# Kernel optimization log

Measured on AMD Instinct MI355X. Metric: run time of the kernel, lower is better.

Reference implementation:

```python
import jax, jax.numpy as jnp
import numpy as np
from jax import lax

N = 163840      # total nodes
E = 2621440     # total edges (avg degree 16)
B = 4096        # number of graphs / batch
F_XD = 78       # node feature dim
L_XT = 735      # cell-line sequence length (gives 2944 after conv/pool stack)


def _params(key):
    ks = jax.random.split(key, 26)
    s = 0.05
    rn = lambda k, sh: (jax.random.normal(k, sh, jnp.float32) * s)
    p = {}
    p['W1'], p['b1'] = rn(ks[0], (78, 78)), rn(ks[1], (78,))
    p['W2'], p['b2'] = rn(ks[2], (78, 156)), rn(ks[3], (156,))
    p['W3'], p['b3'] = rn(ks[4], (156, 312)), rn(ks[5], (312,))
    p['Wg1'], p['bg1'] = rn(ks[6], (312, 1024)), rn(ks[7], (1024,))
    p['Wg2'], p['bg2'] = rn(ks[8], (1024, 128)), rn(ks[9], (128,))
    p['k1'], p['kb1'] = rn(ks[10], (32, 1, 8)), rn(ks[11], (32,))
    p['k2'], p['kb2'] = rn(ks[12], (64, 32, 8)), rn(ks[13], (64,))
    p['k3'], p['kb3'] = rn(ks[14], (128, 64, 8)), rn(ks[15], (128,))
    p['Wxt'], p['bxt'] = rn(ks[16], (2944, 128)), rn(ks[17], (128,))
    p['Wf1'], p['bf1'] = rn(ks[18], (256, 1024)), rn(ks[19], (1024,))
    p['Wf2'], p['bf2'] = rn(ks[20], (1024, 128)), rn(ks[21], (128,))
    p['Wo'], p['bo'] = rn(ks[22], (128, 1)), rn(ks[23], (1,))
    return p


def setup_inputs() -> dict:
    key = jax.random.key(0)
    k0, k1, k2, kp = jax.random.split(key, 4)
    inp = {
        'x': jax.random.normal(k0, (N, F_XD), jnp.float32),
        'edge_index': jax.random.randint(k1, (2, E), 0, N),
        'batch': jnp.arange(N) // (N // B),  # contiguous graph ids, 40 nodes/graph
        'xo': jax.random.normal(k2, (B, 1, L_XT), jnp.float32),
    }
    inp.update(_params(kp))
    return inp


def _forward(x, xo, W1, b1, W2, b2, W3, b3, Wg1, bg1, Wg2, bg2,
             k1, kb1, k2, kb2, k3, kb3, Wxt, bxt, Wf1, bf1, Wf2, bf2, Wo, bo,
             edge_index, batch):
    src, dst = edge_index[0], edge_index[1]
    # GCN symmetric norm with self-loops: deg = in-degree + 1
    deg = jax.ops.segment_sum(jnp.ones(src.shape[0], x.dtype), dst, num_segments=N) + 1.0
    dinv = lax.rsqrt(deg)
    enorm = (dinv[src] * dinv[dst])[:, None]     # [E,1]
    selfn = (dinv * dinv)[:, None]               # [N,1]

    def gcn(h, W, b):
        h = h @ W
        agg = jax.ops.segment_sum(h[src] * enorm, dst, num_segments=N)
        return agg + h * selfn + b

    h = jax.nn.relu(gcn(x, W1, b1))
    h = jax.nn.relu(gcn(h, W2, b2))
    h = jax.nn.relu(gcn(h, W3, b3))
    g = jax.ops.segment_max(h, batch, num_segments=B)   # global max pool -> [B,312]
    g = jax.nn.relu(g @ Wg1 + bg1)
    g = g @ Wg2 + bg2                                   # [B,128] (dropout = eval no-op)

    def conv1d(v, w, b):
        y = lax.conv_general_dilated(v, w, (1,), 'VALID',
                                     dimension_numbers=('NCH', 'OIH', 'NCH'))
        return y + b[None, :, None]

    def pool3(v):
        return lax.reduce_window(v, -jnp.inf, lax.max, (1, 1, 3), (1, 1, 3), 'VALID')

    t = pool3(jax.nn.relu(conv1d(xo, k1, kb1)))   # [B,32,242]
    t = pool3(jax.nn.relu(conv1d(t, k2, kb2)))    # [B,64,78]
    t = pool3(jax.nn.relu(conv1d(t, k3, kb3)))    # [B,128,23]
    t = t.reshape(B, -1) @ Wxt + bxt              # [B,128]

    c = jnp.concatenate([g, t], axis=1)           # [B,256]
    c = jax.nn.relu(c @ Wf1 + bf1)
    c = jax.nn.relu(c @ Wf2 + bf2)
    return c @ Wo + bo                            # [B,1]


def reference(x, edge_index, batch, xo, W1, b1, W2, b2, W3, b3, Wg1, bg1,
              Wg2, bg2, k1, kb1, k2, kb2, k3, kb3, Wxt, bxt, Wf1, bf1,
              Wf2, bf2, Wo, bo):
    return _forward(x, xo, W1, b1, W2, b2, W3, b3, Wg1, bg1, Wg2, bg2,
                    k1, kb1, k2, kb2, k3, kb3, Wxt, bxt, Wf1, bf1, Wf2, bf2,
                    Wo, bo, edge_index, batch)
```

## Files before the change

kernel.cpp:

```cpp
#include <hip/hip_runtime.h>
#include <hip/hip_bf16.h>

#define N_NODES 163840
#define N_EDGES 2621440
#define NB      4096

typedef __hip_bfloat16 bf16;
typedef __attribute__((ext_vector_type(8))) short short8;
typedef __attribute__((ext_vector_type(4))) float floatx4;

__device__ inline float tofloat(float v) { return v; }
__device__ inline float tofloat(bf16 v) { return __bfloat162float(v); }
__device__ inline void storev(float* p, float v) { *p = v; }
__device__ inline void storev(bf16* p, float v) { *p = __float2bfloat16(v); }
__device__ inline float s2f(short s) {
  union { unsigned u; float f; } cv;
  cv.u = ((unsigned)(unsigned short)s) << 16;
  return cv.f;
}
__device__ inline short f2s(float f) {
  bf16 b = __float2bfloat16(f);
  return *(short*)&b;
}


__global__ __launch_bounds__(256) void count_kernel(const int* __restrict__ ei,
                                                    int* __restrict__ indeg) {
  int e = blockIdx.x * 256 + threadIdx.x;
  if (e < N_EDGES) atomicAdd(&indeg[ei[N_EDGES + e]], 1);
}

__global__ __launch_bounds__(256) void scan1_kernel(const int* __restrict__ indeg,
                                                    int* __restrict__ rowstart,
                                                    int* __restrict__ bsums,
                                                    float* __restrict__ dinv) {
  __shared__ int s[256];
  int tid = threadIdx.x;
  int i = blockIdx.x * 256 + tid;
  int v = indeg[i];
  dinv[i] = rsqrtf((float)v + 1.0f);
  s[tid] = v;
  __syncthreads();
  for (int off = 1; off < 256; off <<= 1) {
    int x = (tid >= off) ? s[tid - off] : 0;
    __syncthreads();
    s[tid] += x;
    __syncthreads();
  }
  rowstart[i] = s[tid] - v;
  if (tid == 255) bsums[blockIdx.x] = s[255];
}

__global__ __launch_bounds__(640) void scan2_kernel(const int* __restrict__ bsums,
                                                    int* __restrict__ boffs,
                                                    int* __restrict__ rowstart) {
  __shared__ int s[640];
  int tid = threadIdx.x;
  int v = bsums[tid];
  s[tid] = v;
  __syncthreads();
  for (int off = 1; off < 640; off <<= 1) {
    int x = (tid >= off) ? s[tid - off] : 0;
    __syncthreads();
    s[tid] += x;
    __syncthreads();
  }
  boffs[tid] = s[tid] - v;
  if (tid == 639) rowstart[N_NODES] = s[639];
}

__global__ __launch_bounds__(256) void scan3_kernel(int* __restrict__ rowstart,
                                                    int* __restrict__ cursor,
                                                    const int* __restrict__ boffs) {
  int i = blockIdx.x * 256 + threadIdx.x;
  int v = rowstart[i] + boffs[blockIdx.x];
  rowstart[i] = v;
  cursor[i] = v;
}

__global__ __launch_bounds__(256) void scatter_kernel(const int* __restrict__ ei,
                                                      int* __restrict__ cursor,
                                                      int* __restrict__ csr_src) {
  int e = blockIdx.x * 256 + threadIdx.x;
  int lo = blockIdx.y * (N_NODES / 4);
  int hi = lo + (N_NODES / 4);
  if (e < N_EDGES) {
    int d = ei[N_EDGES + e];
    if (d >= lo && d < hi) {
      int pos = atomicAdd(&cursor[d], 1);
      csr_src[pos] = ei[e];
    }
  }
}

__global__ __launch_bounds__(256) void cast_scale_kernel(const float* __restrict__ x,
                                                         const float* __restrict__ dinv,
                                                         bf16* __restrict__ xb) {
  int i = blockIdx.x * 256 + threadIdx.x;
  if (i < N_NODES * 80) {
    int n = i / 80, f = i - n * 80;
    float v = (f < 78) ? x[n * 78 + f] * dinv[n] : 0.f;
    xb[i] = __float2bfloat16(v);
  }
}

__global__ __launch_bounds__(256) void agg80_kernel(const bf16* __restrict__ hs,
                                                    const float* __restrict__ dinv,
                                                    const int* __restrict__ rowstart,
                                                    const int* __restrict__ csr,
                                                    bf16* __restrict__ out) {
  int node = blockIdx.x * 4 + (threadIdx.x >> 6);
  int lane = threadIdx.x & 63;
  int grp = lane / 10;
  int sub = lane - grp * 10;
  bool active = grp < 6;
  int st = rowstart[node], en = rowstart[node + 1];
  int cnt = en - st + 1;
  float dn = dinv[node];
  float acc[8];
#pragma unroll
  for (int j = 0; j < 8; j++) acc[j] = 0.f;
  for (int e = 0; e < cnt; e += 6) {
    int ri = e + grp;
    bool valid = active && (ri < cnt);
    int cidx = st + ri;
    cidx = (cidx < en) ? cidx : 0;
    int row = (ri < cnt - 1) ? csr[cidx] : node;
    const short* rp = (const short*)hs + (size_t)row * 80 + sub * 8;
    short8 d = *(const short8*)rp;
    float m = valid ? 1.f : 0.f;
#pragma unroll
    for (int j = 0; j < 8; j++) acc[j] += m * s2f(d[j]);
  }
  short ob[8];
#pragma unroll
  for (int j = 0; j < 8; j++) {
    float v = acc[j];
    float t = 0.f;
#pragma unroll
    for (int g = 0; g < 6; g++) t += __shfl(v, sub + 10 * g);
    ob[j] = f2s(t * dn);
  }
  if (grp == 0) {
    short8 pk;
#pragma unroll
    for (int j = 0; j < 8; j++) pk[j] = ob[j];
    *(short8*)((short*)out + (size_t)node * 80 + sub * 8) = pk;
  }
}

__global__ __launch_bounds__(256) void agg192_kernel(const bf16* __restrict__ hs,
                                                     const float* __restrict__ dinv,
                                                     const int* __restrict__ rowstart,
                                                     const int* __restrict__ csr,
                                                     bf16* __restrict__ out) {
  int node = blockIdx.x * 4 + (threadIdx.x >> 6);
  int lane = threadIdx.x & 63;
  int grp = lane >> 3;
  int sub = lane & 7;
  int st = rowstart[node], en = rowstart[node + 1];
  int cnt = en - st + 1;
  float dn = dinv[node];
  float acc[3][8];
#pragma unroll
  for (int k = 0; k < 3; k++)
#pragma unroll
    for (int j = 0; j < 8; j++) acc[k][j] = 0.f;
  for (int e = 0; e < cnt; e += 8) {
    int ri = e + grp;
    bool valid = ri < cnt;
    int cidx = st + ri;
    cidx = (cidx < en) ? cidx : 0;
    int row = (ri < cnt - 1) ? csr[cidx] : node;
    const short* rp = (const short*)hs + (size_t)row * 192 + sub * 8;
    float m = valid ? 1.f : 0.f;
#pragma unroll
    for (int k = 0; k < 3; k++) {
      short8 d = *(const short8*)(rp + k * 64);
#pragma unroll
      for (int j = 0; j < 8; j++) acc[k][j] += m * s2f(d[j]);
    }
  }
#pragma unroll
  for (int k = 0; k < 3; k++) {
    short8 pk;
#pragma unroll
    for (int j = 0; j < 8; j++) {
      float v = acc[k][j];
      v += __shfl_xor(v, 8);
      v += __shfl_xor(v, 16);
      v += __shfl_xor(v, 32);
      pk[j] = f2s(v * dn);
    }
    if (grp == 0 && (k < 2 || sub < 4))
      *(short8*)((short*)out + (size_t)node * 160 + k * 64 + sub * 8) = pk;
  }
}

template <int NT, typename TC>
__global__ __launch_bounds__(256) void gemm_mfma_kernel(
    const bf16* __restrict__ A, const bf16* __restrict__ Bt,
    const float* __restrict__ bias, const float* __restrict__ rowScale,
    TC* __restrict__ C, int M, int Nc, int ncstore, int Ksteps, int lda,
    int kpad, int ldc, int coff, int doRelu) {
  int tid = threadIdx.x;
  int w = tid >> 6, lane = tid & 63;
  int quad = lane >> 4, l16 = lane & 15;
  int r0 = blockIdx.x * 64 + w * 16;
  int c0 = blockIdx.y * (NT * 16);
  floatx4 acc[NT];
#pragma unroll
  for (int t = 0; t < NT; t++) acc[t] = (floatx4){0.f, 0.f, 0.f, 0.f};
  const short* Ap = (const short*)A + (size_t)(r0 + l16) * lda + quad * 8;
  const short* Bp = (const short*)Bt + (size_t)(c0 + l16) * kpad + quad * 8;
  for (int s = 0; s < Ksteps; s++) {
    short8 a = *(const short8*)(Ap + s * 32);
#pragma unroll
    for (int t = 0; t < NT; t++) {
      short8 b = *(const short8*)(Bp + (size_t)t * 16 * kpad + s * 32);
      acc[t] = __builtin_amdgcn_mfma_f32_16x16x32_bf16(a, b, acc[t], 0, 0, 0);
    }
  }
#pragma unroll
  for (int t = 0; t < NT; t++) {
    int c = c0 + t * 16 + l16;
    if (c >= ncstore) continue;
    bool valid = c < Nc;
    float bb = (bias && valid) ? bias[c] : 0.f;
#pragma unroll
    for (int r = 0; r < 4; r++) {
      int row = r0 + quad * 4 + r;
      float v = valid ? acc[t][r] + bb : 0.f;
      if (doRelu) v = fmaxf(v, 0.f);
      if (rowScale) v *= rowScale[row];
      storev(&C[(size_t)row * ldc + coff + c], v);
    }
  }
}

__device__ inline void wtrans_one(const float* __restrict__ W, bf16* __restrict__ Bt,
                                  int K, int N, int Kpad, int idx) {
  int n = idx / Kpad, k = idx - n * Kpad;
  float v = (k < K && n < N) ? W[(size_t)k * N + n] : 0.f;
  Bt[idx] = __float2bfloat16(v);
}
template <int CI, int NCO>
__device__ inline void wprep_one(const float* __restrict__ kw, bf16* __restrict__ Wr,
                                 int idx) {
  int co = idx % NCO, k = idx / NCO;
  int dl = k / CI, ci = k % CI;
  Wr[idx] = __float2bfloat16(kw[(co * CI + ci) * 8 + dl]);
}
__global__ __launch_bounds__(256) void wprep_all_kernel(
    const float* k2, const float* k3, const float* W1, const float* W2,
    const float* W3, const float* Wg1, const float* Wg2, const float* Wxt,
    const float* Wf1, const float* Wf2, bf16* Wr2, bf16* Wr3, bf16* Btw1,
    bf16* Btw2, bf16* BtW3, bf16* Btg1, bf16* Btg2, bf16* Btxt, bf16* Btf1,
    bf16* Btf2, int* indeg) {
  int idx = blockIdx.x * 256 + threadIdx.x;
  if (idx < N_NODES) { indeg[idx] = 0; return; }
  idx -= N_NODES;
  if (idx < 16384) { wprep_one<32, 64>(k2, Wr2, idx); return; }
  idx -= 16384;
  if (idx < 65536) { wprep_one<64, 128>(k3, Wr3, idx); return; }
  idx -= 65536;
  if (idx < 7680) { wtrans_one(W1, Btw1, 78, 78, 96, idx); return; }
  idx -= 7680;
  if (idx < 15360) { wtrans_one(W2, Btw2, 78, 156, 96, idx); return; }
  idx -= 15360;
  if (idx < 51200) { wtrans_one(W3, BtW3, 156, 312, 160, idx); return; }
  idx -= 51200;
  if (idx < 327680) { wtrans_one(Wg1, Btg1, 312, 1024, 320, idx); return; }
  idx -= 327680;
  if (idx < 131072) { wtrans_one(Wg2, Btg2, 1024, 128, 1024, idx); return; }
  idx -= 131072;
  if (idx < 376832) {
    int o = idx / 2944, k = idx - o * 2944;
    int l = k >> 7, co = k & 127;
    Btxt[idx] = __float2bfloat16(Wxt[((size_t)(co * 23 + l)) * 128 + o]);
    return;
  }
  idx -= 376832;
  if (idx < 262144) { wtrans_one(Wf1, Btf1, 256, 1024, 256, idx); return; }
  idx -= 262144;
  if (idx < 131072) { wtrans_one(Wf2, Btf2, 1024, 128, 1024, idx); return; }
}
#define WPREP_TOTAL (N_NODES + 16384 + 65536 + 7680 + 15360 + 51200 + 327680 + 131072 + 376832 + 262144 + 131072)

__global__ __launch_bounds__(256) void gcn3_segmax_mfma_kernel(
    const bf16* __restrict__ agg2, const bf16* __restrict__ BtW3,
    const float* __restrict__ b3, bf16* __restrict__ g) {
  __shared__ __align__(16) bf16 a_lds[160 * 168];
  int tid = threadIdx.x;
  int w = tid >> 6, lane = tid & 63;
  int quad = lane >> 4, l16 = lane & 15;
  int g0 = blockIdx.x * 4;

  short8 bfrag[5][5];
  const short* Bp = (const short*)BtW3 + (size_t)(w * 80 + l16) * 160 + quad * 8;
#pragma unroll
  for (int nt = 0; nt < 5; nt++)
#pragma unroll
    for (int ks = 0; ks < 5; ks++)
      bfrag[nt][ks] = *(const short8*)(Bp + (size_t)nt * 16 * 160 + ks * 32);

  const bf16* src = agg2 + (size_t)g0 * 40 * 160;
  for (int i = tid; i < 160 * 160 / 8; i += 256) {
    int flat = i * 8;
    int row = flat / 160, k = flat - row * 160;
    *(short8*)&a_lds[row * 168 + k] = *(const short8*)&src[flat];
  }
  __syncthreads();

  float gmax[5][4];
#pragma unroll
  for (int nt = 0; nt < 5; nt++)
#pragma unroll
    for (int gi = 0; gi < 4; gi++) gmax[nt][gi] = -3.0e38f;

#pragma unroll
  for (int mt = 0; mt < 10; mt++) {
    floatx4 acc[5];
#pragma unroll
    for (int nt = 0; nt < 5; nt++) acc[nt] = (floatx4){0.f, 0.f, 0.f, 0.f};
#pragma unroll
    for (int ks = 0; ks < 5; ks++) {
      short8 a = *(const short8*)&a_lds[(16 * mt + l16) * 168 + ks * 32 + quad * 8];
#pragma unroll
      for (int nt = 0; nt < 5; nt++)
        acc[nt] = __builtin_amdgcn_mfma_f32_16x16x32_bf16(a, bfrag[nt][ks], acc[nt], 0, 0, 0);
    }
    int gl = (16 * mt + quad * 4) / 40;
#pragma unroll
    for (int nt = 0; nt < 5; nt++) {
      float m4 = fmaxf(fmaxf(acc[nt][0], acc[nt][1]), fmaxf(acc[nt][2], acc[nt][3]));
#pragma unroll
      for (int gi = 0; gi < 4; gi++)
        if (gl == gi) gmax[nt][gi] = fmaxf(gmax[nt][gi], m4);
    }
  }

#pragma unroll
  for (int nt = 0; nt < 5; nt++) {
#pragma unroll
    for (int gi = 0; gi < 4; gi++) {
      float v = gmax[nt][gi];
      v = fmaxf(v, __shfl_xor(v, 16));
      v = fmaxf(v, __shfl_xor(v, 32));
      gmax[nt][gi] = v;
    }
    int c = w * 80 + nt * 16 + l16;
    float bb = (c < 312) ? b3[c] : 0.f;
    float val = fmaxf(gmax[nt][quad] + bb, 0.f);
    g[(size_t)(g0 + quad) * 320 + c] = __float2bfloat16(val);
  }
}

__global__ __launch_bounds__(256) void conv12_kernel(const float* __restrict__ xo,
                                                     const float* __restrict__ k1,
                                                     const float* __restrict__ kb1,
                                                     const bf16* __restrict__ Wr2,
                                                     const float* __restrict__ kb2,
                                                     bf16* __restrict__ outp) {
  constexpr int LPAD = 248, MT = 15, LOUT = 78, G = 2, NCO = 64, CIP = 40;
  __shared__ __align__(16) bf16 lds_in[G * LPAD * CIP];
  __shared__ bf16 stg[4][MT * 16][16];
  __shared__ float xo_s[G][736];
  __shared__ float k1w[256];
  __shared__ float kb1s[32];
  int tid = threadIdx.x;
  int w = tid >> 6, lane = tid & 63;
  int quad = lane >> 4, l16 = lane & 15;
  int bg = blockIdx.x;
  int co0 = w * 16;

  short8 bfrag[8];
#pragma unroll
  for (int s = 0; s < 8; s++) {
#pragma unroll
    for (int j = 0; j < 8; j++) {
      int k = s * 32 + quad * 8 + j;
      bfrag[s][j] = ((const short*)Wr2)[k * NCO + co0 + l16];
    }
  }

  for (int i = tid; i < G * 735; i += 256)
    xo_s[i / 735][i % 735] = xo[(size_t)(bg * G + i / 735) * 735 + i % 735];
  k1w[tid] = k1[tid];
  if (tid < 32) kb1s[tid] = kb1[tid];
  __syncthreads();

  for (int idx = tid; idx < G * 242 * 32; idx += 256) {
    int g = idx / (242 * 32);
    int rem = idx - g * (242 * 32);
    int l = rem >> 5, co = rem & 31;
    int base = l * 3;
    float bs = kb1s[co];
    float a0 = bs, a1 = bs, a2 = bs;
#pragma unroll
    for (int k = 0; k < 8; k++) {
      float wv = k1w[co * 8 + k];
      a0 += wv * xo_s[g][base + k];
      a1 += wv * xo_s[g][base + 1 + k];
      a2 += wv * xo_s[g][base + 2 + k];
    }
    lds_in[(g * LPAD + l) * CIP + co] =
        __float2bfloat16(fmaxf(0.f, fmaxf(a0, fmaxf(a1, a2))));
  }
  for (int i = tid; i < G * 6 * 32; i += 256) {
    int g = i / (6 * 32);
    int rem = i - g * (6 * 32);
    int r = rem >> 5, c = rem & 31;
    lds_in[(g * LPAD + 242 + r) * CIP + c] = __float2bfloat16(0.f);
  }
  __syncthreads();

  for (int g = 0; g < G; g++) {
    const bf16* base = &lds_in[g * LPAD * CIP];
#pragma unroll
    for (int mt = 0; mt < MT; mt++) {
      floatx4 acc = {0.f, 0.f, 0.f, 0.f};
      int m = mt * 16 + l16;
#pragma unroll
      for (int s = 0; s < 8; s++) {
        int kg0 = s * 32 + quad * 8;
        int dl = kg0 >> 5;
        int ci0 = kg0 & 31;
        short8 a = *(const short8*)&base[(m + dl) * CIP + ci0];
        acc = __builtin_amdgcn_mfma_f32_16x16x32_bf16(a, bfrag[s], acc, 0, 0, 0);
      }
#pragma unroll
      for (int r = 0; r < 4; r++)
        stg[w][mt * 16 + quad * 4 + r][l16] = __float2bfloat16(acc[r]);
    }
    __syncthreads();
    float bias = kb2[co0 + l16];
    for (int it = lane; it < LOUT * 16; it += 64) {
      int l = it >> 4;
      float v0 = __bfloat162float(stg[w][3 * l][l16]);
      float v1 = __bfloat162float(stg[w][3 * l + 1][l16]);
      float v2 = __bfloat162float(stg[w][3 * l + 2][l16]);
      float v = fmaxf(fmaxf(v0, v1), v2) + bias;
      outp[((size_t)(bg * G + g) * LOUT + l) * NCO + co0 + l16] =
          __float2bfloat16(fmaxf(v, 0.f));
    }
    __syncthreads();
  }
}

template <int CI, int LIN, int LPAD, int MT, int LOUT, int G, int NCO>
__global__ __launch_bounds__(256) void convmfma_kernel(const bf16* __restrict__ in,
                                                       const bf16* __restrict__ Wr,
                                                       const float* __restrict__ kb,
                                                       bf16* __restrict__ outp) {
  constexpr int KSTEPS = 8 * CI / 32;
  constexpr int CIP = CI + 8;
  __shared__ __align__(16) bf16 lds_in[G * LPAD * CIP];
  __shared__ bf16 stg[4][MT * 16][16];
  int tid = threadIdx.x;
  int w = tid >> 6, lane = tid & 63;
  int quad = lane >> 4, l16 = lane & 15;
  int bg = blockIdx.x;
  int co0 = blockIdx.y * 64 + w * 16;

  short8 bfrag[KSTEPS];
#pragma unroll
  for (int s = 0; s < KSTEPS; s++) {
#pragma unroll
    for (int j = 0; j < 8; j++) {
      int k = s * 32 + quad * 8 + j;
      bfrag[s][j] = ((const short*)Wr)[k * NCO + co0 + l16];
    }
  }

  const bf16* gin = in + (size_t)bg * G * LIN * CI;
  constexpr int NELEM = G * LIN * CI;
  for (int i = tid; i < NELEM / 8; i += 256) {
    int flat = i * 8;
    int g = flat / (LIN * CI);
    int rem = flat - g * (LIN * CI);
    int row = rem / CI, ci = rem - row * CI;
    *(short8*)&lds_in[(g * LPAD + row) * CIP + ci] = *(const short8*)&gin[flat];
  }
  constexpr int PADE = G * (LPAD - LIN) * CIP;
  for (int i = tid; i < PADE / 8; i += 256) {
    int flat = i * 8;
    int g = flat / ((LPAD - LIN) * CIP);
    int rem = flat - g * ((LPAD - LIN) * CIP);
    short8 z = {0, 0, 0, 0, 0, 0, 0, 0};
    *(short8*)&lds_in[(g * LPAD + LIN) * CIP + rem] = z;
  }
  __syncthreads();

  for (int g = 0; g < G; g++) {
    const bf16* base = &lds_in[g * LPAD * CIP];
#pragma unroll
    for (int mt = 0; mt < MT; mt++) {
      floatx4 acc = {0.f, 0.f, 0.f, 0.f};
      int m = mt * 16 + l16;
#pragma unroll
      for (int s = 0; s < KSTEPS; s++) {
        int kg0 = s * 32 + quad * 8;
        int dl = kg0 / CI;
        int ci0 = kg0 % CI;
        short8 a = *(const short8*)&base[(m + dl) * CIP + ci0];
        acc = __builtin_amdgcn_mfma_f32_16x16x32_bf16(a, bfrag[s], acc, 0, 0, 0);
      }
#pragma unroll
      for (int r = 0; r < 4; r++)
        stg[w][mt * 16 + quad * 4 + r][l16] = __float2bfloat16(acc[r]);
    }
    __syncthreads();
    float bias = kb[co0 + l16];
    for (int it = lane; it < LOUT * 16; it += 64) {
      int l = it >> 4;
      float v0 = __bfloat162float(stg[w][3 * l][l16]);
      float v1 = __bfloat162float(stg[w][3 * l + 1][l16]);
      float v2 = __bfloat162float(stg[w][3 * l + 2][l16]);
      float v = fmaxf(fmaxf(v0, v1), v2) + bias;
      outp[((size_t)(bg * G + g) * LOUT + l) * NCO + co0 + l16] =
          __float2bfloat16(fmaxf(v, 0.f));
    }
    __syncthreads();
  }
}

__global__ __launch_bounds__(256) void final_kernel(const float* __restrict__ f2,
                                                    const float* __restrict__ Wo,
                                                    const float* __restrict__ bo,
                                                    float* __restrict__ out) {
  int wid = (blockIdx.x * blockDim.x + threadIdx.x) >> 6;
  int lane = threadIdx.x & 63;
  if (wid >= NB) return;
  float s = f2[wid * 128 + lane] * Wo[lane] + f2[wid * 128 + 64 + lane] * Wo[64 + lane];
  for (int o = 32; o > 0; o >>= 1) s += __shfl_down(s, o);
  if (lane == 0) out[wid] = s + bo[0];
}

extern "C" void kernel_launch(void* const* d_in, const int* in_sizes, int n_in,
                              void* d_out, int out_size, void* d_ws, size_t ws_size,
                              hipStream_t stream) {
  const float* x   = (const float*)d_in[0];
  const int*   ei  = (const int*)d_in[1];
  const float* xo  = (const float*)d_in[3];
  const float* W1  = (const float*)d_in[4];  const float* b1  = (const float*)d_in[5];
  const float* W2  = (const float*)d_in[6];  const float* b2  = (const float*)d_in[7];
  const float* W3  = (const float*)d_in[8];  const float* b3  = (const float*)d_in[9];
  const float* Wg1 = (const float*)d_in[10]; const float* bg1 = (const float*)d_in[11];
  const float* Wg2 = (const float*)d_in[12]; const float* bg2 = (const float*)d_in[13];
  const float* k1  = (const float*)d_in[14]; const float* kb1 = (const float*)d_in[15];
  const float* k2  = (const float*)d_in[16]; const float* kb2 = (const float*)d_in[17];
  const float* k3  = (const float*)d_in[18]; const float* kb3 = (const float*)d_in[19];
  const float* Wxt = (const float*)d_in[20]; const float* bxt = (const float*)d_in[21];
  const float* Wf1 = (const float*)d_in[22]; const float* bf1 = (const float*)d_in[23];
  const float* Wf2 = (const float*)d_in[24]; const float* bf2 = (const float*)d_in[25];
  const float* Wo  = (const float*)d_in[26]; const float* bo  = (const float*)d_in[27];
  float* out = (float*)d_out;

  char* ws = (char*)d_ws;
  size_t off = 0;
  auto alloc = [&](size_t bytes) -> void* {
    void* p = ws + off;
    off += (bytes + 255) & ~(size_t)255;
    return p;
  };

  int*   indeg   = (int*)alloc((size_t)N_NODES * 4);
  float* dinv    = (float*)alloc((size_t)N_NODES * 4);
  int*   rowstart= (int*)alloc((size_t)(N_NODES + 1) * 4);
  int*   cursor  = (int*)alloc((size_t)N_NODES * 4);
  int*   bsums   = (int*)alloc(640 * 4);
  int*   boffs   = (int*)alloc(640 * 4);
  int*   csr     = (int*)alloc((size_t)N_EDGES * 4 + 256);
  bf16*  nb1     = (bf16*)alloc((size_t)N_NODES * 160 * 2);
  bf16*  nb2     = (bf16*)alloc((size_t)NB * 7744 * 2);
  bf16*  gb      = (bf16*)alloc((size_t)NB * 320 * 2);
  bf16*  g1b     = (bf16*)alloc((size_t)NB * 1024 * 2);
  bf16*  gtb     = (bf16*)alloc((size_t)NB * 256 * 2);
  float* f2      = (float*)alloc((size_t)NB * 128 * 4);
  bf16*  Wr2     = (bf16*)alloc((size_t)256 * 64 * 2);
  bf16*  Wr3     = (bf16*)alloc((size_t)512 * 128 * 2);
  bf16*  Btw1    = (bf16*)alloc((size_t)80 * 96 * 2);
  bf16*  Btw2    = (bf16*)alloc((size_t)160 * 96 * 2);
  bf16*  BtW3    = (bf16*)alloc((size_t)320 * 160 * 2);
  bf16*  Btg1    = (bf16*)alloc((size_t)1024 * 320 * 2);
  bf16*  Btg2    = (bf16*)alloc((size_t)128 * 1024 * 2);
  bf16*  Btxt    = (bf16*)alloc((size_t)128 * 2944 * 2);
  bf16*  Btf1    = (bf16*)alloc((size_t)1024 * 256 * 2);
  bf16*  Btf2    = (bf16*)alloc((size_t)128 * 1024 * 2);

  bf16* xb  = nb2;
  bf16* h   = nb2;
  bf16* ag  = nb1;
  bf16* c2  = nb1;
  bf16* c3  = nb2;
  bf16* f1b = g1b;

  wprep_all_kernel<<<(WPREP_TOTAL + 255) / 256, 256, 0, stream>>>(
      k2, k3, W1, W2, W3, Wg1, Wg2, Wxt, Wf1, Wf2, Wr2, Wr3, Btw1, Btw2, BtW3,
      Btg1, Btg2, Btxt, Btf1, Btf2, indeg);

  count_kernel<<<N_EDGES / 256, 256, 0, stream>>>(ei, indeg);
  scan1_kernel<<<640, 256, 0, stream>>>(indeg, rowstart, bsums, dinv);
  scan2_kernel<<<1, 640, 0, stream>>>(bsums, boffs, rowstart);
  scan3_kernel<<<640, 256, 0, stream>>>(rowstart, cursor, boffs);
  scatter_kernel<<<dim3(N_EDGES / 256, 4), 256, 0, stream>>>(ei, cursor, csr);

  cast_scale_kernel<<<(N_NODES * 80 + 255) / 256, 256, 0, stream>>>(x, dinv, xb);
  agg80_kernel<<<N_NODES / 4, 256, 0, stream>>>(xb, dinv, rowstart, csr, ag);
  gemm_mfma_kernel<5, bf16><<<dim3(N_NODES / 64, 1), 256, 0, stream>>>(
      ag, Btw1, b1, dinv, h, N_NODES, 78, 80, 3, 80, 96, 80, 0, 1);
  agg80_kernel<<<N_NODES / 4, 256, 0, stream>>>(h, dinv, rowstart, csr, ag);
  gemm_mfma_kernel<6, bf16><<<dim3(N_NODES / 64, 2), 256, 0, stream>>>(
      ag, Btw2, b2, dinv, h, N_NODES, 156, 192, 3, 80, 96, 192, 0, 1);
  agg192_kernel<<<N_NODES / 4, 256, 0, stream>>>(h, dinv, rowstart, csr, ag);
  gcn3_segmax_mfma_kernel<<<NB / 4, 256, 0, stream>>>(ag, BtW3, b3, gb);

  gemm_mfma_kernel<4, bf16><<<dim3(NB / 64, 16), 256, 0, stream>>>(
      gb, Btg1, bg1, nullptr, g1b, NB, 1024, 1024, 10, 320, 320, 1024, 0, 1);
  gemm_mfma_kernel<4, bf16><<<dim3(NB / 64, 2), 256, 0, stream>>>(
      g1b, Btg2, bg2, nullptr, gtb, NB, 128, 128, 32, 1024, 1024, 256, 0, 0);

  conv12_kernel<<<NB / 2, 256, 0, stream>>>(xo, k1, kb1, Wr2, kb2, c2);
  convmfma_kernel<64, 78, 88, 5, 23, 4, 128>
      <<<dim3(NB / 4, 2), 256, 0, stream>>>(c2, Wr3, kb3, c3);
  gemm_mfma_kernel<4, bf16><<<dim3(NB / 64, 2), 256, 0, stream>>>(
      c3, Btxt, bxt, nullptr, gtb, NB, 128, 128, 92, 2944, 2944, 256, 128, 0);

  gemm_mfma_kernel<4, bf16><<<dim3(NB / 64, 16), 256, 0, stream>>>(
      gtb, Btf1, bf1, nullptr, f1b, NB, 1024, 1024, 8, 256, 256, 1024, 0, 1);
  gemm_mfma_kernel<4, float><<<dim3(NB / 64, 2), 256, 0, stream>>>(
      f1b, Btf2, bf2, nullptr, f2, NB, 128, 128, 32, 1024, 1024, 128, 0, 1);
  final_kernel<<<NB * 64 / 256, 256, 0, stream>>>(f2, Wo, bo, out);
}
```

Baseline: 1.166 ms.

## Fuse GCN neighbor aggregation with the following MFMA GEMM for layers 1-2

Replaces separate agg80 and gemm kernels for the first two GCN layers with one kernel. Each wave aggregates 16 nodes into shared memory, then runs the small 80-wide MFMA GEMM with bias, ReLU and dinv scaling directly from LDS. This removes the round-trip of the aggregated features through global memory and two kernel launches. In exchange each wave processes 16 nodes sequentially, which lowers the parallelism available to hide gather latency, and the per-node grid of 40960 blocks becomes 2560 blocks.

```diff
diff --git a/kernel.cpp b/kernel.cpp
--- a/kernel.cpp
+++ b/kernel.cpp
@@ -104,48 +104,79 @@
   }
 }
 
-__global__ __launch_bounds__(256) void agg80_kernel(const bf16* __restrict__ hs,
-                                                    const float* __restrict__ dinv,
-                                                    const int* __restrict__ rowstart,
-                                                    const int* __restrict__ csr,
-                                                    bf16* __restrict__ out) {
-  int node = blockIdx.x * 4 + (threadIdx.x >> 6);
-  int lane = threadIdx.x & 63;
-  int grp = lane / 10;
-  int sub = lane - grp * 10;
+template <int NT>
+__global__ __launch_bounds__(256) void gcn_fused_kernel(
+    const bf16* __restrict__ hs, const float* __restrict__ dinv,
+    const int* __restrict__ rowstart, const int* __restrict__ csr,
+    const bf16* __restrict__ Bt, const float* __restrict__ bias,
+    bf16* __restrict__ hout, int Nc, int ldc) {
+  __shared__ __align__(16) bf16 a_s[64 * 88 + 8];
+  int tid = threadIdx.x;
+  int w = tid >> 6, lane = tid & 63;
+  int quad = lane >> 4, l16 = lane & 15;
+  int grp = lane / 10, sub = lane - grp * 10;
   bool active = grp < 6;
-  int st = rowstart[node], en = rowstart[node + 1];
-  int cnt = en - st + 1;
-  float dn = dinv[node];
-  float acc[8];
-#pragma unroll
-  for (int j = 0; j < 8; j++) acc[j] = 0.f;
-  for (int e = 0; e < cnt; e += 6) {
-    int ri = e + grp;
-    bool valid = active && (ri < cnt);
-    int cidx = st + ri;
-    cidx = (cidx < en) ? cidx : 0;
-    int row = (ri < cnt - 1) ? csr[cidx] : node;
-    const short* rp = (const short*)hs + (size_t)row * 80 + sub * 8;
-    short8 d = *(const short8*)rp;
-    float m = valid ? 1.f : 0.f;
-#pragma unroll
-    for (int j = 0; j < 8; j++) acc[j] += m * s2f(d[j]);
-  }
-  short ob[8];
-#pragma unroll
-  for (int j = 0; j < 8; j++) {
-    float v = acc[j];
-    float t = 0.f;
-#pragma unroll
-    for (int g = 0; g < 6; g++) t += __shfl(v, sub + 10 * g);
-    ob[j] = f2s(t * dn);
-  }
-  if (grp == 0) {
+  int nbase = blockIdx.x * 64 + w * 16;
+
+  for (int t = 0; t < 16; t++) {
+    int node = nbase + t;
+    int st = rowstart[node], en = rowstart[node + 1];
+    int cnt = en - st + 1;
+    float acc[8];
+#pragma unroll
+    for (int j = 0; j < 8; j++) acc[j] = 0.f;
+    for (int e = 0; e < cnt; e += 6) {
+      int ri = e + grp;
+      bool valid = active && (ri < cnt);
+      int cidx = st + ri;
+      cidx = (cidx < en) ? cidx : 0;
+      int row = (ri < cnt - 1) ? csr[cidx] : node;
+      const short* rp = (const short*)hs + (size_t)row * 80 + sub * 8;
+      short8 d = *(const short8*)rp;
+      float m = valid ? 1.f : 0.f;
+#pragma unroll
+      for (int j = 0; j < 8; j++) acc[j] += m * s2f(d[j]);
+    }
+    float dn = dinv[node];
     short8 pk;
 #pragma unroll
-    for (int j = 0; j < 8; j++) pk[j] = ob[j];
-    *(short8*)((short*)out + (size_t)node * 80 + sub * 8) = pk;
+    for (int j = 0; j < 8; j++) {
+      float v = acc[j];
+      float s = 0.f;
+#pragma unroll
+      for (int g = 0; g < 6; g++) s += __shfl(v, sub + 10 * g);
+      pk[j] = f2s(s * dn);
+    }
+    if (grp == 0)
+      *(short8*)&a_s[(w * 16 + t) * 88 + sub * 8] = pk;
+  }
+
+  floatx4 acc2[NT];
+#pragma unroll
+  for (int t = 0; t < NT; t++) acc2[t] = (floatx4){0.f, 0.f, 0.f, 0.f};
+  const short* Ap = (const short*)&a_s[(w * 16 + l16) * 88 + quad * 8];
+  const short* Bp = (const short*)Bt + (size_t)l16 * 96 + quad * 8;
+#pragma unroll
+  for (int s = 0; s < 3; s++) {
+    short8 a = *(const short8*)(Ap + s * 32);
+#pragma unroll
+    for (int t = 0; t < NT; t++) {
+      short8 b = *(const short8*)(Bp + (size_t)t * 16 * 96 + s * 32);
+      acc2[t] = __builtin_amdgcn_mfma_f32_16x16x32_bf16(a, b, acc2[t], 0, 0, 0);
+    }
+  }
+#pragma unroll
+  for (int t = 0; t < NT; t++) {
+    int c = t * 16 + l16;
+    bool valid = c < Nc;
+    float bb = valid ? bias[c] : 0.f;
+#pragma unroll
+    for (int r = 0; r < 4; r++) {
+      int row = nbase + quad * 4 + r;
+      float v = valid ? acc2[t][r] + bb : 0.f;
+      v = fmaxf(v, 0.f) * dinv[row];
+      storev(&hout[(size_t)row * ldc + c], v);
+    }
   }
 }
 
@@ -590,8 +621,9 @@
   bf16*  Btf2    = (bf16*)alloc((size_t)128 * 1024 * 2);
 
   bf16* xb  = nb2;
-  bf16* h   = nb2;
-  bf16* ag  = nb1;
+  bf16* h1  = nb1;
+  bf16* h2  = nb2;
+  bf16* ag2 = nb1;
   bf16* c2  = nb1;
   bf16* c3  = nb2;
   bf16* f1b = g1b;
@@ -607,14 +639,12 @@
   scatter_kernel<<<dim3(N_EDGES / 256, 4), 256, 0, stream>>>(ei, cursor, csr);
 
   cast_scale_kernel<<<(N_NODES * 80 + 255) / 256, 256, 0, stream>>>(x, dinv, xb);
-  agg80_kernel<<<N_NODES / 4, 256, 0, stream>>>(xb, dinv, rowstart, csr, ag);
-  gemm_mfma_kernel<5, bf16><<<dim3(N_NODES / 64, 1), 256, 0, stream>>>(
-      ag, Btw1, b1, dinv, h, N_NODES, 78, 80, 3, 80, 96, 80, 0, 1);
-  agg80_kernel<<<N_NODES / 4, 256, 0, stream>>>(h, dinv, rowstart, csr, ag);
-  gemm_mfma_kernel<6, bf16><<<dim3(N_NODES / 64, 2), 256, 0, stream>>>(
-      ag, Btw2, b2, dinv, h, N_NODES, 156, 192, 3, 80, 96, 192, 0, 1);
-  agg192_kernel<<<N_NODES / 4, 256, 0, stream>>>(h, dinv, rowstart, csr, ag);
-  gcn3_segmax_mfma_kernel<<<NB / 4, 256, 0, stream>>>(ag, BtW3, b3, gb);
+  gcn_fused_kernel<5><<<N_NODES / 64, 256, 0, stream>>>(
+      xb, dinv, rowstart, csr, Btw1, b1, h1, 78, 80);
+  gcn_fused_kernel<12><<<N_NODES / 64, 256, 0, stream>>>(
+      h1, dinv, rowstart, csr, Btw2, b2, h2, 156, 192);
+  agg192_kernel<<<N_NODES / 4, 256, 0, stream>>>(h2, dinv, rowstart, csr, ag2);
+  gcn3_segmax_mfma_kernel<<<NB / 4, 256, 0, stream>>>(ag2, BtW3, b3, gb);
 
   gemm_mfma_kernel<4, bf16><<<dim3(NB / 64, 16), 256, 0, stream>>>(
       gb, Btg1, bg1, nullptr, g1b, NB, 1024, 1024, 10, 320, 320, 1024, 0, 1);
```

Measured after the change: 1.250 ms. 1.07x slower.
